# Performance work log

Measured on AMD Instinct MI355X. Metric: run time of the kernel, lower is better.

The kernel has to match this reference:

```python
import jax, jax.numpy as jnp
import numpy as np

SLICES = [(12, 1), (13, 1)]  # (input_width, hidden_size=1) per slice


def _lstm_last_hidden(xs, W_ih, W_hh, b):
    """Run a standard (PyTorch gate order i,f,g,o) LSTM over time, return last h.
    xs: [T, B, in]; W_ih: [4*H, in]; W_hh: [4*H, H]; b: [4*H] (b_ih + b_hh).
    Returns h_T: [B, H].
    """
    B = xs.shape[1]
    H = W_hh.shape[1]
    h0 = jnp.zeros((B, H), xs.dtype)
    c0 = jnp.zeros((B, H), xs.dtype)

    def step(carry, xt):
        h, c = carry
        gates = xt @ W_ih.T + h @ W_hh.T + b  # [B, 4H]
        i, f, g, o = jnp.split(gates, 4, axis=-1)
        i = jax.nn.sigmoid(i)
        f = jax.nn.sigmoid(f)
        g = jnp.tanh(g)
        o = jax.nn.sigmoid(o)
        c = f * c + i * g
        h = o * jnp.tanh(c)
        return (h, c), None

    (hT, _), _ = jax.lax.scan(step, (h0, c0), xs)
    return hT


def setup_inputs() -> dict:
    key = jax.random.key(0)
    ks = jax.random.split(key, 9)
    B, T, F = 4096, 512, 25
    nb_out = 1
    s = 0.1
    x = jax.random.normal(ks[0], (B, T, F), dtype=jnp.float32)
    # slice-1 LSTM (input 12, hidden 1)
    W_ih1 = jax.random.normal(ks[1], (4, 12), dtype=jnp.float32) * s
    W_hh1 = jax.random.normal(ks[2], (4, 1), dtype=jnp.float32) * s
    b1 = jax.random.normal(ks[3], (4,), dtype=jnp.float32) * s
    # slice-2 LSTM (input 13, hidden 1)
    W_ih2 = jax.random.normal(ks[4], (4, 13), dtype=jnp.float32) * s
    W_hh2 = jax.random.normal(ks[5], (4, 1), dtype=jnp.float32) * s
    b2 = jax.random.normal(ks[6], (4,), dtype=jnp.float32) * s
    # output head Linear(2, nb_out)
    W_out = jax.random.normal(ks[7], (nb_out, 2), dtype=jnp.float32) * s
    b_out = jax.random.normal(ks[8], (nb_out,), dtype=jnp.float32) * s
    return {"x": x, "W_ih1": W_ih1, "W_hh1": W_hh1, "b1": b1,
            "W_ih2": W_ih2, "W_hh2": W_hh2, "b2": b2,
            "W_out": W_out, "b_out": b_out}


def reference(x, W_ih1, W_hh1, b1, W_ih2, W_hh2, b2, W_out, b_out):
    # x: [B, T, 25] -> time-major [T, B, 25]
    xs = jnp.transpose(x, (1, 0, 2))
    h1 = _lstm_last_hidden(xs[..., :12], W_ih1, W_hh1, b1)   # [B, 1]
    h2 = _lstm_last_hidden(xs[..., 12:], W_ih2, W_hh2, b2)   # [B, 1]
    h = jnp.concatenate([h1, h2], axis=-1)                   # [B, 2] == lstm_out[:, -1, :]
    out = h @ W_out.T + b_out                                # [B, nb_out]
    return jax.nn.sigmoid(out)
```

## Files before the change

kernel.cpp:

```cpp
#include <hip/hip_runtime.h>
#include <stdint.h>


#define T_STEPS 512
#define F_IN    25
#define TC      16
#define NTILES  (T_STEPS / TC)
#define CH      8
#define XROW    520
#define ZROW    (TC * 8 + 8)
#define LOG2E   1.44269504088896340736f

typedef const __attribute__((address_space(1))) void* as1_cvp;
typedef __attribute__((address_space(3)))       void* as3_vp;

__device__ __forceinline__ void gll16(const float* gsrc, const float* ldst) {
  __builtin_amdgcn_global_load_lds((as1_cvp)(uintptr_t)gsrc,
                                   (as3_vp)(uint32_t)(uintptr_t)ldst, 16, 0, 0);
}

__device__ __forceinline__ float sigm(float v) {
  return __builtin_amdgcn_rcpf(1.0f + __builtin_amdgcn_exp2f(v * (-LOG2E)));
}
__device__ __forceinline__ float tanh_(float v) {
  return fmaf(2.0f, __builtin_amdgcn_rcpf(1.0f + __builtin_amdgcn_exp2f(v * (-2.0f * LOG2E))), -1.0f);
}

__device__ __forceinline__ void prefetch_tile(const float* __restrict__ x, int b0, int tile,
                                              float* xbuf, int lane) {
  const float* base = x + (size_t)b0 * (T_STEPS * F_IN) + tile * (TC * F_IN);
  const int i1 = lane * 4;
  int i2 = 256 + lane * 4;
  if (i2 > 396) i2 = 396;
#pragma unroll
  for (int cc = 0; cc < CH; ++cc) {
    const float* g0 = base + cc * (T_STEPS * F_IN);
    gll16(g0 + i1, xbuf + cc * XROW);
    gll16(g0 + i2, xbuf + cc * XROW + 256);
  }
}

__device__ __forceinline__ void gemv_tile(const float* __restrict__ xbuf, float* __restrict__ zbuf,
                                          int c, int lt,
                                          const float* __restrict__ w1, const float* __restrict__ w2,
                                          const float* __restrict__ zb) {
#pragma unroll
  for (int p = 0; p < 2; ++p) {
    const int tl = p * 8 + lt;
    const float* xr = xbuf + c * XROW + tl * F_IN;
    float z[8];
#pragma unroll
    for (int j = 0; j < 8; ++j) z[j] = zb[j];
#pragma unroll
    for (int f = 0; f < 12; ++f) {
      const float xv = xr[f];
#pragma unroll
      for (int j = 0; j < 4; ++j) z[j] = fmaf(w1[j * 12 + f], xv, z[j]);
    }
#pragma unroll
    for (int f = 0; f < 13; ++f) {
      const float xv = xr[12 + f];
#pragma unroll
      for (int j = 0; j < 4; ++j) z[4 + j] = fmaf(w2[j * 13 + f], xv, z[4 + j]);
    }
    float4* zp = (float4*)(zbuf + c * ZROW + tl * 8);
    zp[0] = make_float4(z[0], z[1], z[2], z[3]);
    zp[1] = make_float4(z[4], z[5], z[6], z[7]);
  }
}

__device__ __forceinline__ void scan_tile(const float* __restrict__ zbuf, int c, int zoff,
                                          const float* __restrict__ whh, float& hv, float& cv) {
#pragma unroll
  for (int t = 0; t < TC; ++t) {
    const float4 z4 = *(const float4*)(zbuf + c * ZROW + t * 8 + zoff);
    const float pi = fmaf(hv, whh[0], z4.x);
    const float pf = fmaf(hv, whh[1], z4.y);
    const float pg = fmaf(hv, whh[2], z4.z);
    const float po = fmaf(hv, whh[3], z4.w);
    const float ai = sigm(pi);
    const float af = sigm(pf);
    const float ag = tanh_(pg);
    const float ao = sigm(po);
    cv = fmaf(af, cv, ai * ag);
    hv = ao * tanh_(cv);
  }
}

__global__ void __launch_bounds__(64, 1)
lstm2_fused(const float* __restrict__ x,
            const float* __restrict__ Wih1, const float* __restrict__ Whh1, const float* __restrict__ b1,
            const float* __restrict__ Wih2, const float* __restrict__ Whh2, const float* __restrict__ b2,
            const float* __restrict__ Wout, const float* __restrict__ bout,
            float* __restrict__ out)
{
  __shared__ __align__(16) float xs0[CH * XROW];
  __shared__ __align__(16) float xs1[CH * XROW];
  __shared__ __align__(16) float zs0[CH * ZROW];
  __shared__ __align__(16) float zs1[CH * ZROW];

  const int lane = threadIdx.x;
  const int c    = lane >> 3;
  const int g    = lane & 7;
  const int b0   = blockIdx.x * CH;
  const int zoff = g & 4;

  float w1[48], w2[52], zb[8], whh[4];
#pragma unroll
  for (int j = 0; j < 48; ++j) w1[j] = Wih1[j];
#pragma unroll
  for (int j = 0; j < 52; ++j) w2[j] = Wih2[j];
#pragma unroll
  for (int j = 0; j < 4; ++j) { zb[j] = b1[j]; zb[4 + j] = b2[j]; }
#pragma unroll
  for (int j = 0; j < 4; ++j) whh[j] = (g < 4) ? Whh1[j] : Whh2[j];

  float hv = 0.0f, cv = 0.0f;

  prefetch_tile(x, b0, 0, xs0, lane);
  asm volatile("s_waitcnt vmcnt(0)" ::: "memory");
  prefetch_tile(x, b0, 1, xs1, lane);
  gemv_tile(xs0, zs0, c, g, w1, w2, zb);
  asm volatile("s_waitcnt lgkmcnt(0)" ::: "memory");

  for (int k = 0; k < NTILES - 1; ++k) {
    asm volatile("s_waitcnt vmcnt(0)" ::: "memory");
    int tn = k + 2;
    if (tn > NTILES - 1) tn = NTILES - 1;
    prefetch_tile(x, b0, tn, (k & 1) ? xs1 : xs0, lane);
    const float* zrd = (k & 1) ? zs1 : zs0;
    const float* xrd = (k & 1) ? xs0 : xs1;
    float*       zwr = (k & 1) ? zs0 : zs1;
    scan_tile(zrd, c, zoff, whh, hv, cv);
    gemv_tile(xrd, zwr, c, g, w1, w2, zb);
    asm volatile("s_waitcnt lgkmcnt(0)" ::: "memory");
  }
  scan_tile(zs1, c, zoff, whh, hv, cv);

  const float h1 = __shfl(hv, (lane & 56) + 0, 64);
  const float h2 = __shfl(hv, (lane & 56) + 4, 64);
  if (g == 0) {
    out[b0 + c] = sigm(fmaf(Wout[0], h1, fmaf(Wout[1], h2, bout[0])));
  }
}

extern "C" void kernel_launch(void* const* d_in, const int* in_sizes, int n_in,
                              void* d_out, int out_size, void* d_ws, size_t ws_size,
                              hipStream_t stream) {
  const float* x    = (const float*)d_in[0];
  const float* Wih1 = (const float*)d_in[1];
  const float* Whh1 = (const float*)d_in[2];
  const float* b1   = (const float*)d_in[3];
  const float* Wih2 = (const float*)d_in[4];
  const float* Whh2 = (const float*)d_in[5];
  const float* b2   = (const float*)d_in[6];
  const float* Wout = (const float*)d_in[7];
  const float* bout = (const float*)d_in[8];
  float* out = (float*)d_out;

  const int B = in_sizes[0] / (T_STEPS * F_IN);
  dim3 grid(B / CH), block(64);
  hipLaunchKernelGGL(lstm2_fused, grid, block, 0, stream,
                     x, Wih1, Whh1, b1, Wih2, Whh2, b2, Wout, bout, out);
}
```

Baseline: 306.5 us.

## Split LSTM into parallel gate-projection kernel and lean recurrent scan kernel

```diff
diff --git a/kernel.cpp b/kernel.cpp
--- a/kernel.cpp
+++ b/kernel.cpp
@@ -4,12 +4,13 @@
 
 #define T_STEPS 512
 #define F_IN    25
-#define TC      16
-#define NTILES  (T_STEPS / TC)
+#define TC      32
+#define NT1     (T_STEPS / TC)
 #define CH      8
-#define XROW    520
-#define ZROW    (TC * 8 + 8)
+#define TILE_F  (CH * TC * F_IN)
 #define LOG2E   1.44269504088896340736f
+#define SC1     (-LOG2E)
+#define SC2     (-2.0f * LOG2E)
 
 typedef const __attribute__((address_space(1))) void* as1_cvp;
 typedef __attribute__((address_space(3)))       void* as3_vp;
@@ -19,128 +20,134 @@
                                    (as3_vp)(uint32_t)(uintptr_t)ldst, 16, 0, 0);
 }
 
-__device__ __forceinline__ float sigm(float v) {
-  return __builtin_amdgcn_rcpf(1.0f + __builtin_amdgcn_exp2f(v * (-LOG2E)));
-}
-__device__ __forceinline__ float tanh_(float v) {
-  return fmaf(2.0f, __builtin_amdgcn_rcpf(1.0f + __builtin_amdgcn_exp2f(v * (-2.0f * LOG2E))), -1.0f);
-}
+__global__ void __launch_bounds__(256, 2)
+k1_gates(const float* __restrict__ x,
+         const float* __restrict__ Wih1, const float* __restrict__ b1,
+         const float* __restrict__ Wih2, const float* __restrict__ b2,
+         float* __restrict__ z, int B)
+{
+  __shared__ __align__(16) float xs[2 * TILE_F];
 
-__device__ __forceinline__ void prefetch_tile(const float* __restrict__ x, int b0, int tile,
-                                              float* xbuf, int lane) {
-  const float* base = x + (size_t)b0 * (T_STEPS * F_IN) + tile * (TC * F_IN);
-  const int i1 = lane * 4;
-  int i2 = 256 + lane * 4;
-  if (i2 > 396) i2 = 396;
+  const int tid  = threadIdx.x;
+  const int wv   = tid >> 6;
+  const int lane = tid & 63;
+  const int b0   = blockIdx.x * CH;
+
+  const float* gp[7];
+  int ioff[7];
 #pragma unroll
-  for (int cc = 0; cc < CH; ++cc) {
-    const float* g0 = base + cc * (T_STEPS * F_IN);
-    gll16(g0 + i1, xbuf + cc * XROW);
-    gll16(g0 + i2, xbuf + cc * XROW + 256);
+  for (int j = 0; j < 7; ++j) {
+    const int i = wv + 4 * j;
+    if (i < 25) {
+      const int F = i * 256 + lane * 4;
+      const int c = F / (TC * F_IN);
+      const int r = F - c * (TC * F_IN);
+      gp[j]   = x + (size_t)(b0 + c) * (T_STEPS * F_IN) + r;
+      ioff[j] = i * 256;
+    } else { gp[j] = x; ioff[j] = -1; }
   }
-}
 
-__device__ __forceinline__ void gemv_tile(const float* __restrict__ xbuf, float* __restrict__ zbuf,
-                                          int c, int lt,
-                                          const float* __restrict__ w1, const float* __restrict__ w2,
-                                          const float* __restrict__ zb) {
+  const int c  = tid >> 5;
+  const int tl = tid & 31;
+
 #pragma unroll
-  for (int p = 0; p < 2; ++p) {
-    const int tl = p * 8 + lt;
-    const float* xr = xbuf + c * XROW + tl * F_IN;
-    float z[8];
+  for (int j = 0; j < 7; ++j)
+    if (ioff[j] >= 0) gll16(gp[j], xs + ioff[j]);
+  __syncthreads();
+
+  float4* __restrict__ z4 = (float4*)z;
+
+  for (int k = 0; k < NT1; ++k) {
+    if (k + 1 < NT1) {
+      const int h = (k + 1) & 1;
 #pragma unroll
-    for (int j = 0; j < 8; ++j) z[j] = zb[j];
+      for (int j = 0; j < 7; ++j)
+        if (ioff[j] >= 0) gll16(gp[j] + (k + 1) * (TC * F_IN), xs + h * TILE_F + ioff[j]);
+    }
+
+    const float* xr = xs + (k & 1) * TILE_F + c * (TC * F_IN) + tl * F_IN;
+    float zz[8];
+#pragma unroll
+    for (int j = 0; j < 4; ++j) { zz[j] = b1[j]; zz[4 + j] = b2[j]; }
 #pragma unroll
     for (int f = 0; f < 12; ++f) {
       const float xv = xr[f];
 #pragma unroll
-      for (int j = 0; j < 4; ++j) z[j] = fmaf(w1[j * 12 + f], xv, z[j]);
+      for (int j = 0; j < 4; ++j) zz[j] = fmaf(Wih1[j * 12 + f], xv, zz[j]);
     }
 #pragma unroll
     for (int f = 0; f < 13; ++f) {
       const float xv = xr[12 + f];
 #pragma unroll
-      for (int j = 0; j < 4; ++j) z[4 + j] = fmaf(w2[j * 13 + f], xv, z[4 + j]);
+      for (int j = 0; j < 4; ++j) zz[4 + j] = fmaf(Wih2[j * 13 + f], xv, zz[4 + j]);
     }
-    float4* zp = (float4*)(zbuf + c * ZROW + tl * 8);
-    zp[0] = make_float4(z[0], z[1], z[2], z[3]);
-    zp[1] = make_float4(z[4], z[5], z[6], z[7]);
+    const float4 q0 = make_float4(zz[0] * SC1, zz[1] * SC1, zz[2] * SC2, zz[3] * SC1);
+    const float4 q1 = make_float4(zz[4] * SC1, zz[5] * SC1, zz[6] * SC2, zz[7] * SC1);
+    const size_t idx = (size_t)(k * TC + tl) * B + (b0 + c);
+    z4[idx * 2]     = q0;
+    z4[idx * 2 + 1] = q1;
+
+    __syncthreads();
   }
 }
 
-__device__ __forceinline__ void scan_tile(const float* __restrict__ zbuf, int c, int zoff,
-                                          const float* __restrict__ whh, float& hv, float& cv) {
-#pragma unroll
-  for (int t = 0; t < TC; ++t) {
-    const float4 z4 = *(const float4*)(zbuf + c * ZROW + t * 8 + zoff);
-    const float pi = fmaf(hv, whh[0], z4.x);
-    const float pf = fmaf(hv, whh[1], z4.y);
-    const float pg = fmaf(hv, whh[2], z4.z);
-    const float po = fmaf(hv, whh[3], z4.w);
-    const float ai = sigm(pi);
-    const float af = sigm(pf);
-    const float ag = tanh_(pg);
-    const float ao = sigm(po);
-    cv = fmaf(af, cv, ai * ag);
-    hv = ao * tanh_(cv);
-  }
+__device__ __forceinline__ void lstm_step(const float4 zv,
+                                          const float wi, const float wf,
+                                          const float wg, const float wo,
+                                          float& h, float& cc) {
+  const float ei = __builtin_amdgcn_exp2f(fmaf(h, wi, zv.x));
+  const float ef = __builtin_amdgcn_exp2f(fmaf(h, wf, zv.y));
+  const float eg = __builtin_amdgcn_exp2f(fmaf(h, wg, zv.z));
+  const float eo = __builtin_amdgcn_exp2f(fmaf(h, wo, zv.w));
+  const float af  = __builtin_amdgcn_rcpf(1.0f + ef);
+  const float rig = __builtin_amdgcn_rcpf((1.0f + ei) * (1.0f + eg));
+  const float ig  = (1.0f - eg) * rig;
+  cc = fmaf(af, cc, ig);
+  const float ec  = __builtin_amdgcn_exp2f(cc * SC2);
+  const float roc = __builtin_amdgcn_rcpf((1.0f + eo) * (1.0f + ec));
+  h = (1.0f - ec) * roc;
 }
 
 __global__ void __launch_bounds__(64, 1)
-lstm2_fused(const float* __restrict__ x,
-            const float* __restrict__ Wih1, const float* __restrict__ Whh1, const float* __restrict__ b1,
-            const float* __restrict__ Wih2, const float* __restrict__ Whh2, const float* __restrict__ b2,
-            const float* __restrict__ Wout, const float* __restrict__ bout,
-            float* __restrict__ out)
+k2_scan(const float* __restrict__ z,
+        const float* __restrict__ Whh1, const float* __restrict__ Whh2,
+        const float* __restrict__ Wout, const float* __restrict__ bout,
+        float* __restrict__ out, int B)
 {
-  __shared__ __align__(16) float xs0[CH * XROW];
-  __shared__ __align__(16) float xs1[CH * XROW];
-  __shared__ __align__(16) float zs0[CH * ZROW];
-  __shared__ __align__(16) float zs1[CH * ZROW];
+  const int l    = threadIdx.x;
+  const int bb   = blockIdx.x * 32 + (l >> 1);
+  const int lstm = l & 1;
 
-  const int lane = threadIdx.x;
-  const int c    = lane >> 3;
-  const int g    = lane & 7;
-  const int b0   = blockIdx.x * CH;
-  const int zoff = g & 4;
+  const float* wp = lstm ? Whh2 : Whh1;
+  const float wi = SC1 * wp[0];
+  const float wf = SC1 * wp[1];
+  const float wg = SC2 * wp[2];
+  const float wo = SC1 * wp[3];
 
-  float w1[48], w2[52], zb[8], whh[4];
+  const float4* __restrict__ zp = (const float4*)z;
+  const size_t stride = (size_t)B * 2;
+  const size_t base   = (size_t)bb * 2 + lstm;
+
+  float4 rb[8];
 #pragma unroll
-  for (int j = 0; j < 48; ++j) w1[j] = Wih1[j];
+  for (int j = 0; j < 8; ++j) rb[j] = zp[(size_t)j * stride + base];
+
+  float h = 0.0f, cc = 0.0f;
+
+  for (int t0 = 0; t0 < T_STEPS - 8; t0 += 8) {
 #pragma unroll
-  for (int j = 0; j < 52; ++j) w2[j] = Wih2[j];
+    for (int j = 0; j < 8; ++j) {
+      lstm_step(rb[j], wi, wf, wg, wo, h, cc);
+      rb[j] = zp[(size_t)(t0 + j + 8) * stride + base];
+    }
+  }
 #pragma unroll
-  for (int j = 0; j < 4; ++j) { zb[j] = b1[j]; zb[4 + j] = b2[j]; }
-#pragma unroll
-  for (int j = 0; j < 4; ++j) whh[j] = (g < 4) ? Whh1[j] : Whh2[j];
+  for (int j = 0; j < 8; ++j) lstm_step(rb[j], wi, wf, wg, wo, h, cc);
 
-  float hv = 0.0f, cv = 0.0f;
-
-  prefetch_tile(x, b0, 0, xs0, lane);
-  asm volatile("s_waitcnt vmcnt(0)" ::: "memory");
-  prefetch_tile(x, b0, 1, xs1, lane);
-  gemv_tile(xs0, zs0, c, g, w1, w2, zb);
-  asm volatile("s_waitcnt lgkmcnt(0)" ::: "memory");
-
-  for (int k = 0; k < NTILES - 1; ++k) {
-    asm volatile("s_waitcnt vmcnt(0)" ::: "memory");
-    int tn = k + 2;
-    if (tn > NTILES - 1) tn = NTILES - 1;
-    prefetch_tile(x, b0, tn, (k & 1) ? xs1 : xs0, lane);
-    const float* zrd = (k & 1) ? zs1 : zs0;
-    const float* xrd = (k & 1) ? xs0 : xs1;
-    float*       zwr = (k & 1) ? zs0 : zs1;
-    scan_tile(zrd, c, zoff, whh, hv, cv);
-    gemv_tile(xrd, zwr, c, g, w1, w2, zb);
-    asm volatile("s_waitcnt lgkmcnt(0)" ::: "memory");
-  }
-  scan_tile(zs1, c, zoff, whh, hv, cv);
-
-  const float h1 = __shfl(hv, (lane & 56) + 0, 64);
-  const float h2 = __shfl(hv, (lane & 56) + 4, 64);
-  if (g == 0) {
-    out[b0 + c] = sigm(fmaf(Wout[0], h1, fmaf(Wout[1], h2, bout[0])));
+  const float hp = __shfl_xor(h, 1);
+  if (lstm == 0) {
+    const float p = fmaf(Wout[0], h, fmaf(Wout[1], hp, bout[0]));
+    out[bb] = __builtin_amdgcn_rcpf(1.0f + __builtin_amdgcn_exp2f(p * SC1));
   }
 }
 
@@ -157,9 +164,12 @@
   const float* Wout = (const float*)d_in[7];
   const float* bout = (const float*)d_in[8];
   float* out = (float*)d_out;
+  float* z   = (float*)d_ws;
 
   const int B = in_sizes[0] / (T_STEPS * F_IN);
-  dim3 grid(B / CH), block(64);
-  hipLaunchKernelGGL(lstm2_fused, grid, block, 0, stream,
-                     x, Wih1, Whh1, b1, Wih2, Whh2, b2, Wout, bout, out);
+
+  hipLaunchKernelGGL(k1_gates, dim3(B / CH), dim3(256), 0, stream,
+                     x, Wih1, b1, Wih2, b2, z, B);
+  hipLaunchKernelGGL(k2_scan, dim3(B / 32), dim3(64), 0, stream,
+                     z, Whh1, Whh2, Wout, bout, out, B);
 }
```

Result: slower. 349.1 us (+13.9%).
